# Kernel tuning notes

Hardware: AMD Instinct MI355X
Metric: run time of the kernel (lower is better)

## Reference

```python
import jax, jax.numpy as jnp
import numpy as np

L, B, D, H = 256, 128, 2048, 2048


def setup_inputs() -> dict:
    key = jax.random.key(0)
    k_x, k_ih, k_hh, k_b = jax.random.split(key, 4)
    scale_ih = 1.0 / np.sqrt(D)
    scale_hh = 1.0 / np.sqrt(H)
    return {
        "inputs": jax.random.normal(k_x, (L, B, D), dtype=jnp.float32),
        "W_ih": jax.random.normal(k_ih, (D, H), dtype=jnp.float32) * scale_ih,
        "W_hh": jax.random.normal(k_hh, (H, H), dtype=jnp.float32) * scale_hh,
        "b": jax.random.normal(k_b, (H,), dtype=jnp.float32) * scale_hh,
    }


def reference(inputs, W_ih, W_hh, b):
    """RNN.forward with a vanilla tanh cell, non-packed path, return_output=True.

    cell.forward(x, h) -> (h', h') with h' = tanh(x @ W_ih + h @ W_hh + b).
    default_state = zeros. Returns (stacked outputs [L,B,H], final state [B,H]).
    """
    # Hoist the input projection out of the scan (x @ W_ih is time-parallel).
    xp = jnp.einsum("lbd,dh->lbh", inputs, W_ih) + b  # [L, B, H]

    def step(h, x_t):
        h_new = jnp.tanh(x_t + h @ W_hh)  # [B, H]
        return h_new, h_new

    h0 = jnp.zeros((inputs.shape[1], W_hh.shape[0]), dtype=inputs.dtype)
    final_state, outputs = jax.lax.scan(step, h0, xp)
    return outputs, final_state
```

## Files before the change

kernel.cpp:

```cpp
#include <hip/hip_runtime.h>
#include <hip/hip_bf16.h>
#include <cmath>

#define LSEQ 256
#define BB   128
#define DD   2048
#define HH   2048
#define LB   (LSEQ * BB)
#define BH   (BB * HH)

typedef __attribute__((ext_vector_type(8))) short bf16x8;
typedef __attribute__((ext_vector_type(4))) float f32x4;

__device__ __forceinline__ void split2(float x, short& hi, short& lo) {
    unsigned u = __float_as_uint(x);
    hi = (short)(u >> 16);
    float r = x - __uint_as_float(u & 0xffff0000u);
    lo = (short)(__float_as_uint(r) >> 16);
}

__global__ __launch_bounds__(256) void xp_gemm(const float* __restrict__ A,
                                               const float* __restrict__ W,
                                               const float* __restrict__ bias,
                                               float* __restrict__ C) {
    __shared__ float As[128][33];
    __shared__ float Bs[128][33];

    const int tid  = threadIdx.x;
    const int lane = tid & 63;
    const int wave = tid >> 6;
    const int wm   = (wave >> 1) * 64;
    const int wn   = (wave & 1) * 64;
    const int l15  = lane & 15;
    const int lk   = (lane >> 4) * 8;

    const int row0 = blockIdx.x * 128;
    const int col0 = blockIdx.y * 128;

    f32x4 acc[4][4] = {};

    const int ar  = tid >> 3;
    const int ac4 = (tid & 7) * 4;
    const int bk  = tid >> 5;
    const int bc4 = (tid & 31) * 4;

    for (int k0 = 0; k0 < DD; k0 += 32) {
#pragma unroll
        for (int i = 0; i < 4; ++i) {
            const float4 v = *reinterpret_cast<const float4*>(
                &A[(size_t)(row0 + ar + 32 * i) * DD + k0 + ac4]);
            As[ar + 32 * i][ac4 + 0] = v.x;
            As[ar + 32 * i][ac4 + 1] = v.y;
            As[ar + 32 * i][ac4 + 2] = v.z;
            As[ar + 32 * i][ac4 + 3] = v.w;
        }
#pragma unroll
        for (int i = 0; i < 4; ++i) {
            const float4 v = *reinterpret_cast<const float4*>(
                &W[(size_t)(k0 + bk + 8 * i) * HH + col0 + bc4]);
            Bs[bc4 + 0][bk + 8 * i] = v.x;
            Bs[bc4 + 1][bk + 8 * i] = v.y;
            Bs[bc4 + 2][bk + 8 * i] = v.z;
            Bs[bc4 + 3][bk + 8 * i] = v.w;
        }
        __syncthreads();

        bf16x8 ah[4], al[4], bh[4], bl[4];
#pragma unroll
        for (int m = 0; m < 4; ++m) {
            const float* p = &As[wm + m * 16 + l15][lk];
#pragma unroll
            for (int j = 0; j < 8; ++j) {
                short h, l;
                split2(p[j], h, l);
                ah[m][j] = h; al[m][j] = l;
            }
        }
#pragma unroll
        for (int n = 0; n < 4; ++n) {
            const float* p = &Bs[wn + n * 16 + l15][lk];
#pragma unroll
            for (int j = 0; j < 8; ++j) {
                short h, l;
                split2(p[j], h, l);
                bh[n][j] = h; bl[n][j] = l;
            }
        }
#pragma unroll
        for (int m = 0; m < 4; ++m)
#pragma unroll
            for (int n = 0; n < 4; ++n) {
                acc[m][n] = __builtin_amdgcn_mfma_f32_16x16x32_bf16(ah[m], bh[n], acc[m][n], 0, 0, 0);
                acc[m][n] = __builtin_amdgcn_mfma_f32_16x16x32_bf16(ah[m], bl[n], acc[m][n], 0, 0, 0);
                acc[m][n] = __builtin_amdgcn_mfma_f32_16x16x32_bf16(al[m], bh[n], acc[m][n], 0, 0, 0);
            }
        __syncthreads();
    }

    const int r4 = (lane >> 4) * 4;
#pragma unroll
    for (int m = 0; m < 4; ++m)
#pragma unroll
        for (int n = 0; n < 4; ++n)
#pragma unroll
            for (int r = 0; r < 4; ++r) {
                const int row = row0 + wm + m * 16 + r4 + r;
                const int col = col0 + wn + n * 16 + l15;
                C[(size_t)row * HH + col] = acc[m][n][r] + bias[col];
            }
}

__global__ __launch_bounds__(256) void tanh0_kernel(float* __restrict__ out0) {
    const int i = blockIdx.x * 256 + threadIdx.x;
    float4* p = reinterpret_cast<float4*>(out0) + i;
    float4 v = *p;
    v.x = tanhf(v.x);
    v.y = tanhf(v.y);
    v.z = tanhf(v.z);
    v.w = tanhf(v.w);
    *p = v;
}

__global__ __launch_bounds__(256) void rnn_step(const float* __restrict__ hprev,
                                                const float* __restrict__ W,
                                                float* __restrict__ io) {
    __shared__ float As[4][32][33];
    __shared__ float Bs[4][32][33];
    __shared__ float red[4][32][33];

    const int tid  = threadIdx.x;
    const int lane = tid & 63;
    const int wave = tid >> 6;
    const int l15  = lane & 15;
    const int lk   = (lane >> 4) * 8;

    const int nc = blockIdx.x & 63;
    const int mr = blockIdx.x >> 6;
    const int m0 = mr * 32;
    const int n0 = nc * 32;

    const int r0 = lane >> 3;
    const int c4 = (lane & 7) * 4;

    f32x4 acc[2][2] = {};

    for (int kt = 0; kt < 16; ++kt) {
        const int k0 = wave * 512 + kt * 32;
#pragma unroll
        for (int i = 0; i < 4; ++i) {
            const float4 v = *reinterpret_cast<const float4*>(
                &hprev[(size_t)(m0 + r0 + 8 * i) * HH + k0 + c4]);
            As[wave][r0 + 8 * i][c4 + 0] = v.x;
            As[wave][r0 + 8 * i][c4 + 1] = v.y;
            As[wave][r0 + 8 * i][c4 + 2] = v.z;
            As[wave][r0 + 8 * i][c4 + 3] = v.w;
        }
#pragma unroll
        for (int i = 0; i < 4; ++i) {
            const float4 v = *reinterpret_cast<const float4*>(
                &W[(size_t)(k0 + r0 + 8 * i) * HH + n0 + c4]);
            Bs[wave][c4 + 0][r0 + 8 * i] = v.x;
            Bs[wave][c4 + 1][r0 + 8 * i] = v.y;
            Bs[wave][c4 + 2][r0 + 8 * i] = v.z;
            Bs[wave][c4 + 3][r0 + 8 * i] = v.w;
        }
        bf16x8 ah[2], al[2], bh[2], bl[2];
#pragma unroll
        for (int m = 0; m < 2; ++m) {
            const float* p = &As[wave][m * 16 + l15][lk];
#pragma unroll
            for (int j = 0; j < 8; ++j) {
                short h, l;
                split2(p[j], h, l);
                ah[m][j] = h; al[m][j] = l;
            }
        }
#pragma unroll
        for (int n = 0; n < 2; ++n) {
            const float* p = &Bs[wave][n * 16 + l15][lk];
#pragma unroll
            for (int j = 0; j < 8; ++j) {
                short h, l;
                split2(p[j], h, l);
                bh[n][j] = h; bl[n][j] = l;
            }
        }
#pragma unroll
        for (int m = 0; m < 2; ++m)
#pragma unroll
            for (int n = 0; n < 2; ++n) {
                acc[m][n] = __builtin_amdgcn_mfma_f32_16x16x32_bf16(ah[m], bh[n], acc[m][n], 0, 0, 0);
                acc[m][n] = __builtin_amdgcn_mfma_f32_16x16x32_bf16(ah[m], bl[n], acc[m][n], 0, 0, 0);
                acc[m][n] = __builtin_amdgcn_mfma_f32_16x16x32_bf16(al[m], bh[n], acc[m][n], 0, 0, 0);
            }
    }

    const int r4 = (lane >> 4) * 4;
#pragma unroll
    for (int m = 0; m < 2; ++m)
#pragma unroll
        for (int n = 0; n < 2; ++n)
#pragma unroll
            for (int r = 0; r < 4; ++r)
                red[wave][m * 16 + r4 + r][n * 16 + l15] = acc[m][n][r];
    __syncthreads();

    const int rr = tid >> 3;
    const int cc = (tid & 7) * 4;
    float* dst = &io[(size_t)(m0 + rr) * HH + n0 + cc];
    float4 xv = *reinterpret_cast<const float4*>(dst);
    float o0 = xv.x + red[0][rr][cc + 0] + red[1][rr][cc + 0] + red[2][rr][cc + 0] + red[3][rr][cc + 0];
    float o1 = xv.y + red[0][rr][cc + 1] + red[1][rr][cc + 1] + red[2][rr][cc + 1] + red[3][rr][cc + 1];
    float o2 = xv.z + red[0][rr][cc + 2] + red[1][rr][cc + 2] + red[2][rr][cc + 2] + red[3][rr][cc + 2];
    float o3 = xv.w + red[0][rr][cc + 3] + red[1][rr][cc + 3] + red[2][rr][cc + 3] + red[3][rr][cc + 3];
    float4 ov;
    ov.x = tanhf(o0);
    ov.y = tanhf(o1);
    ov.z = tanhf(o2);
    ov.w = tanhf(o3);
    *reinterpret_cast<float4*>(dst) = ov;
}

extern "C" void kernel_launch(void* const* d_in, const int* in_sizes, int n_in,
                              void* d_out, int out_size, void* d_ws, size_t ws_size,
                              hipStream_t stream) {
    (void)in_sizes; (void)n_in; (void)d_ws; (void)ws_size; (void)out_size;

    const float* X   = (const float*)d_in[0];
    const float* Wih = (const float*)d_in[1];
    const float* Whh = (const float*)d_in[2];
    const float* b   = (const float*)d_in[3];
    float* out = (float*)d_out;

    dim3 g1(LB / 128, HH / 128);
    xp_gemm<<<g1, 256, 0, stream>>>(X, Wih, b, out);

    tanh0_kernel<<<256, 256, 0, stream>>>(out);

    for (int t = 1; t < LSEQ; ++t) {
        rnn_step<<<256, 256, 0, stream>>>(out + (size_t)(t - 1) * BH, Whh,
                                          out + (size_t)t * BH);
    }

    hipMemcpyAsync(out + (size_t)LSEQ * BH, out + (size_t)(LSEQ - 1) * BH,
                   (size_t)BH * sizeof(float), hipMemcpyDeviceToDevice, stream);
}
```

Before: 5.111 ms.

## Pre-split weights into transposed bf16 hi/lo and carry split hidden state

Adds a pre-pass that transposes W_ih and W_hh and splits them into bf16 hi/lo halves in workspace, so the GEMMs load ready MFMA operands with global_load_lds instead of re-splitting fp32 every tile. The recurrent step now also writes the hi/lo split of the new hidden state into ping-pong buffers, so the next step reads bf16 operands directly. It also changes rnn_step tiling to 64x32 with 128 blocks, swizzles LDS for the input GEMM, and remaps the xp_gemm grid. The cost is two extra transpose kernels, extra global writes of the split state, and fewer blocks per step.

After: 6.997 ms. 36.9% more time.

```diff
diff --git a/kernel.cpp b/kernel.cpp
--- a/kernel.cpp
+++ b/kernel.cpp
@@ -6,10 +6,10 @@
 #define BB   128
 #define DD   2048
 #define HH   2048
-#define LB   (LSEQ * BB)
-#define BH   (BB * HH)
-
-typedef __attribute__((ext_vector_type(8))) short bf16x8;
+#define BH   (BB*HH)
+
+typedef __attribute__((ext_vector_type(8))) short short8;
+typedef __attribute__((ext_vector_type(4))) short short4v;
 typedef __attribute__((ext_vector_type(4))) float f32x4;
 
 __device__ __forceinline__ void split2(float x, short& hi, short& lo) {
@@ -19,72 +19,121 @@
     lo = (short)(__float_as_uint(r) >> 16);
 }
 
-__global__ __launch_bounds__(256) void xp_gemm(const float* __restrict__ A,
-                                               const float* __restrict__ W,
+__device__ __forceinline__ void g2l16(const void* g, void* l) {
+    __builtin_amdgcn_global_load_lds(
+        (const __attribute__((address_space(1))) unsigned int*)g,
+        (__attribute__((address_space(3))) unsigned int*)l, 16, 0, 0);
+}
+
+__global__ __launch_bounds__(256) void transpose_split(const float* __restrict__ W,
+                                                       short* __restrict__ outH,
+                                                       short* __restrict__ outL) {
+    __shared__ float S[64][65];
+    const int tid = threadIdx.x;
+    const int r0 = blockIdx.x * 64;
+    const int c0 = blockIdx.y * 64;
+    const int lr = tid >> 2;
+    const int lc = (tid & 3) * 16;
+#pragma unroll
+    for (int j = 0; j < 4; ++j) {
+        f32x4 v = *(const f32x4*)&W[(size_t)(r0 + lr) * DD + c0 + lc + 4*j];
+#pragma unroll
+        for (int q = 0; q < 4; ++q) S[lr][lc + 4*j + q] = v[q];
+    }
+    __syncthreads();
+    short8 h8[2], l8[2];
+#pragma unroll
+    for (int j = 0; j < 16; ++j) {
+        short h, l;
+        split2(S[lc + j][lr], h, l);
+        h8[j >> 3][j & 7] = h; l8[j >> 3][j & 7] = l;
+    }
+    const size_t o = (size_t)(c0 + lr) * DD + r0 + lc;
+    *(short8*)&outH[o]     = h8[0];
+    *(short8*)&outH[o + 8] = h8[1];
+    *(short8*)&outL[o]     = l8[0];
+    *(short8*)&outL[o + 8] = l8[1];
+}
+
+__global__ __launch_bounds__(256) void xp_gemm(const float* __restrict__ X,
+                                               const short* __restrict__ WTh,
+                                               const short* __restrict__ WTl,
                                                const float* __restrict__ bias,
                                                float* __restrict__ C) {
-    __shared__ float As[128][33];
-    __shared__ float Bs[128][33];
-
-    const int tid  = threadIdx.x;
-    const int lane = tid & 63;
-    const int wave = tid >> 6;
-    const int wm   = (wave >> 1) * 64;
-    const int wn   = (wave & 1) * 64;
-    const int l15  = lane & 15;
-    const int lk   = (lane >> 4) * 8;
-
-    const int row0 = blockIdx.x * 128;
-    const int col0 = blockIdx.y * 128;
+    __shared__ short Ah_s[128*32], Al_s[128*32];
+    __shared__ short Bh_s[128*32], Bl_s[128*32];
+
+    const int tid = threadIdx.x, lane = tid & 63, wave = tid >> 6;
+    const int l15 = lane & 15, lg = lane >> 4;
+
+    const int gid = blockIdx.x;
+    const int rt = ((gid >> 8) << 4) | (gid & 15);
+    const int ct = (gid >> 4) & 15;
+    const int row0 = rt * 128, col0 = ct * 128;
+
+    const int wm = (wave >> 1) * 64, wn = (wave & 1) * 64;
+
+    const int s_row = tid >> 1;
+    const float* gA = X + (size_t)(row0 + s_row) * DD + (tid & 1) * 16;
+    const int swzw = ((s_row >> 1) & 3) << 4;
+    char* pAh0 = (char*)Ah_s + s_row*64 + (((tid & 1)*32 +  0) ^ swzw);
+    char* pAh1 = (char*)Ah_s + s_row*64 + (((tid & 1)*32 + 16) ^ swzw);
+    char* pAl0 = (char*)Al_s + s_row*64 + (((tid & 1)*32 +  0) ^ swzw);
+    char* pAl1 = (char*)Al_s + s_row*64 + (((tid & 1)*32 + 16) ^ swzw);
+
+    const int brow = lane >> 2, bcol = (lane & 3) * 8;
+    const short* gBh = WTh + (size_t)(col0 + wave*32 + brow) * DD + bcol;
+    const short* gBl = WTl + (size_t)(col0 + wave*32 + brow) * DD + bcol;
+    short* lBh = &Bh_s[(wave*32)*32];
+    short* lBl = &Bl_s[(wave*32)*32];
+
+    int ra[4], rb[4];
+#pragma unroll
+    for (int m = 0; m < 4; ++m) {
+        const int rowm = wm + m*16 + l15;
+        ra[m] = rowm*64 + ((lg*16) ^ (((rowm >> 1) & 3) << 4));
+    }
+#pragma unroll
+    for (int n = 0; n < 4; ++n) {
+        const int rn = wn + n*16 + l15;
+        rb[n] = rn*64 + lg*16;
+    }
 
     f32x4 acc[4][4] = {};
 
-    const int ar  = tid >> 3;
-    const int ac4 = (tid & 7) * 4;
-    const int bk  = tid >> 5;
-    const int bc4 = (tid & 31) * 4;
-
     for (int k0 = 0; k0 < DD; k0 += 32) {
-#pragma unroll
-        for (int i = 0; i < 4; ++i) {
-            const float4 v = *reinterpret_cast<const float4*>(
-                &A[(size_t)(row0 + ar + 32 * i) * DD + k0 + ac4]);
-            As[ar + 32 * i][ac4 + 0] = v.x;
-            As[ar + 32 * i][ac4 + 1] = v.y;
-            As[ar + 32 * i][ac4 + 2] = v.z;
-            As[ar + 32 * i][ac4 + 3] = v.w;
-        }
-#pragma unroll
-        for (int i = 0; i < 4; ++i) {
-            const float4 v = *reinterpret_cast<const float4*>(
-                &W[(size_t)(k0 + bk + 8 * i) * HH + col0 + bc4]);
-            Bs[bc4 + 0][bk + 8 * i] = v.x;
-            Bs[bc4 + 1][bk + 8 * i] = v.y;
-            Bs[bc4 + 2][bk + 8 * i] = v.z;
-            Bs[bc4 + 3][bk + 8 * i] = v.w;
-        }
+        float xr[16];
+        *(f32x4*)&xr[0]  = *(const f32x4*)(gA + k0);
+        *(f32x4*)&xr[4]  = *(const f32x4*)(gA + k0 + 4);
+        *(f32x4*)&xr[8]  = *(const f32x4*)(gA + k0 + 8);
+        *(f32x4*)&xr[12] = *(const f32x4*)(gA + k0 + 12);
+
+        g2l16(gBh + k0,          lBh);
+        g2l16(gBh + k0 + 16*DD,  lBh + 16*32);
+        g2l16(gBl + k0,          lBl);
+        g2l16(gBl + k0 + 16*DD,  lBl + 16*32);
+
+        short8 vh0, vh1, vl0, vl1;
+#pragma unroll
+        for (int j = 0; j < 8; ++j) {
+            short h, l;
+            split2(xr[j], h, l);     vh0[j] = h; vl0[j] = l;
+            split2(xr[8+j], h, l);   vh1[j] = h; vl1[j] = l;
+        }
+        *(short8*)pAh0 = vh0; *(short8*)pAh1 = vh1;
+        *(short8*)pAl0 = vl0; *(short8*)pAl1 = vl1;
         __syncthreads();
 
-        bf16x8 ah[4], al[4], bh[4], bl[4];
+        short8 ah[4], al[4], bh[4], bl[4];
 #pragma unroll
         for (int m = 0; m < 4; ++m) {
-            const float* p = &As[wm + m * 16 + l15][lk];
-#pragma unroll
-            for (int j = 0; j < 8; ++j) {
-                short h, l;
-                split2(p[j], h, l);
-                ah[m][j] = h; al[m][j] = l;
-            }
+            ah[m] = *(const short8*)((const char*)Ah_s + ra[m]);
+            al[m] = *(const short8*)((const char*)Al_s + ra[m]);
         }
 #pragma unroll
         for (int n = 0; n < 4; ++n) {
-            const float* p = &Bs[wn + n * 16 + l15][lk];
-#pragma unroll
-            for (int j = 0; j < 8; ++j) {
-                short h, l;
-                split2(p[j], h, l);
-                bh[n][j] = h; bl[n][j] = l;
-            }
+            bh[n] = *(const short8*)((const char*)Bh_s + rb[n]);
+            bl[n] = *(const short8*)((const char*)Bl_s + rb[n]);
         }
 #pragma unroll
         for (int m = 0; m < 4; ++m)
@@ -97,134 +146,140 @@
         __syncthreads();
     }
 
-    const int r4 = (lane >> 4) * 4;
+    float bv[4];
+#pragma unroll
+    for (int n = 0; n < 4; ++n) bv[n] = bias[col0 + wn + n*16 + l15];
 #pragma unroll
     for (int m = 0; m < 4; ++m)
 #pragma unroll
         for (int n = 0; n < 4; ++n)
 #pragma unroll
-            for (int r = 0; r < 4; ++r) {
-                const int row = row0 + wm + m * 16 + r4 + r;
-                const int col = col0 + wn + n * 16 + l15;
-                C[(size_t)row * HH + col] = acc[m][n][r] + bias[col];
+            for (int i = 0; i < 4; ++i) {
+                const int row = row0 + wm + m*16 + lg*4 + i;
+                const int col = col0 + wn + n*16 + l15;
+                C[(size_t)row * HH + col] = acc[m][n][i] + bv[n];
             }
 }
 
-__global__ __launch_bounds__(256) void tanh0_kernel(float* __restrict__ out0) {
+__global__ __launch_bounds__(256) void tanh0_kernel(float* __restrict__ out0,
+                                                    short* __restrict__ oHi,
+                                                    short* __restrict__ oLo) {
     const int i = blockIdx.x * 256 + threadIdx.x;
-    float4* p = reinterpret_cast<float4*>(out0) + i;
-    float4 v = *p;
-    v.x = tanhf(v.x);
-    v.y = tanhf(v.y);
-    v.z = tanhf(v.z);
-    v.w = tanhf(v.w);
-    *p = v;
-}
-
-__global__ __launch_bounds__(256) void rnn_step(const float* __restrict__ hprev,
-                                                const float* __restrict__ W,
-                                                float* __restrict__ io) {
-    __shared__ float As[4][32][33];
-    __shared__ float Bs[4][32][33];
-    __shared__ float red[4][32][33];
-
-    const int tid  = threadIdx.x;
-    const int lane = tid & 63;
-    const int wave = tid >> 6;
-    const int l15  = lane & 15;
-    const int lk   = (lane >> 4) * 8;
-
-    const int nc = blockIdx.x & 63;
-    const int mr = blockIdx.x >> 6;
-    const int m0 = mr * 32;
-    const int n0 = nc * 32;
-
-    const int r0 = lane >> 3;
-    const int c4 = (lane & 7) * 4;
-
-    f32x4 acc[2][2] = {};
+    f32x4 v = ((const f32x4*)out0)[i];
+    short4v h4, l4;
+#pragma unroll
+    for (int q = 0; q < 4; ++q) {
+        const float t = tanhf(v[q]);
+        v[q] = t;
+        short h, l; split2(t, h, l);
+        h4[q] = h; l4[q] = l;
+    }
+    ((f32x4*)out0)[i]   = v;
+    ((short4v*)oHi)[i]  = h4;
+    ((short4v*)oLo)[i]  = l4;
+}
+
+__global__ __launch_bounds__(256) void rnn_step(const short* __restrict__ hHi,
+                                                const short* __restrict__ hLo,
+                                                const short* __restrict__ WTh,
+                                                const short* __restrict__ WTl,
+                                                float* __restrict__ io,
+                                                short* __restrict__ oHi,
+                                                short* __restrict__ oLo) {
+    __shared__ short Ah_s[4][64*32], Al_s[4][64*32];
+    __shared__ short Bh_s[4][32*32], Bl_s[4][32*32];
+    __shared__ float red[4][64*32];
+
+    const int tid = threadIdx.x, lane = tid & 63, wave = tid >> 6;
+    const int l15 = lane & 15, lg = lane >> 4;
+    const int mr = blockIdx.x & 1, nc = blockIdx.x >> 1;
+    const int m0 = mr * 64, n0 = nc * 32;
+
+    const int srow = lane >> 2, scol = (lane & 3) * 8;
+
+    const short* baseAh = hHi + (size_t)(m0 + srow) * HH + scol;
+    const short* baseAl = hLo + (size_t)(m0 + srow) * HH + scol;
+    const short* baseBh = WTh + (size_t)(n0 + srow) * HH + scol;
+    const short* baseBl = WTl + (size_t)(n0 + srow) * HH + scol;
+
+    f32x4 acc[4][2] = {};
 
     for (int kt = 0; kt < 16; ++kt) {
         const int k0 = wave * 512 + kt * 32;
 #pragma unroll
         for (int i = 0; i < 4; ++i) {
-            const float4 v = *reinterpret_cast<const float4*>(
-                &hprev[(size_t)(m0 + r0 + 8 * i) * HH + k0 + c4]);
-            As[wave][r0 + 8 * i][c4 + 0] = v.x;
-            As[wave][r0 + 8 * i][c4 + 1] = v.y;
-            As[wave][r0 + 8 * i][c4 + 2] = v.z;
-            As[wave][r0 + 8 * i][c4 + 3] = v.w;
-        }
-#pragma unroll
-        for (int i = 0; i < 4; ++i) {
-            const float4 v = *reinterpret_cast<const float4*>(
-                &W[(size_t)(k0 + r0 + 8 * i) * HH + n0 + c4]);
-            Bs[wave][c4 + 0][r0 + 8 * i] = v.x;
-            Bs[wave][c4 + 1][r0 + 8 * i] = v.y;
-            Bs[wave][c4 + 2][r0 + 8 * i] = v.z;
-            Bs[wave][c4 + 3][r0 + 8 * i] = v.w;
-        }
-        bf16x8 ah[2], al[2], bh[2], bl[2];
-#pragma unroll
-        for (int m = 0; m < 2; ++m) {
-            const float* p = &As[wave][m * 16 + l15][lk];
-#pragma unroll
-            for (int j = 0; j < 8; ++j) {
-                short h, l;
-                split2(p[j], h, l);
-                ah[m][j] = h; al[m][j] = l;
+            g2l16(baseAh + (size_t)i*16*HH + k0, &Ah_s[wave][i*16*32]);
+            g2l16(baseAl + (size_t)i*16*HH + k0, &Al_s[wave][i*16*32]);
+        }
+#pragma unroll
+        for (int i = 0; i < 2; ++i) {
+            g2l16(baseBh + (size_t)i*16*HH + k0, &Bh_s[wave][i*16*32]);
+            g2l16(baseBl + (size_t)i*16*HH + k0, &Bl_s[wave][i*16*32]);
+        }
+        __syncthreads();
+
+        short8 a_h[4], a_l[4], b_h[2], b_l[2];
+#pragma unroll
+        for (int m = 0; m < 4; ++m) {
+            a_h[m] = *(const short8*)&Ah_s[wave][(m*16 + l15)*32 + lg*8];
+            a_l[m] = *(const short8*)&Al_s[wave][(m*16 + l15)*32 + lg*8];
+        }
+#pragma unroll
+        for (int n = 0; n < 2; ++n) {
+            b_h[n] = *(const short8*)&Bh_s[wave][(n*16 + l15)*32 + lg*8];
+            b_l[n] = *(const short8*)&Bl_s[wave][(n*16 + l15)*32 + lg*8];
+        }
+#pragma unroll
+        for (int m = 0; m < 4; ++m)
+#pragma unroll
+            for (int n = 0; n < 2; ++n) {
+                acc[m][n] = __builtin_amdgcn_mfma_f32_16x16x32_bf16(a_h[m], b_h[n], acc[m][n], 0, 0, 0);
+                acc[m][n] = __builtin_amdgcn_mfma_f32_16x16x32_bf16(a_h[m], b_l[n], acc[m][n], 0, 0, 0);
+                acc[m][n] = __builtin_amdgcn_mfma_f32_16x16x32_bf16(a_l[m], b_h[n], acc[m][n], 0, 0, 0);
             }
-        }
-#pragma unroll
-        for (int n = 0; n < 2; ++n) {
-            const float* p = &Bs[wave][n * 16 + l15][lk];
-#pragma unroll
-            for (int j = 0; j < 8; ++j) {
-                short h, l;
-                split2(p[j], h, l);
-                bh[n][j] = h; bl[n][j] = l;
-            }
-        }
-#pragma unroll
-        for (int m = 0; m < 2; ++m)
-#pragma unroll
-            for (int n = 0; n < 2; ++n) {
-                acc[m][n] = __builtin_amdgcn_mfma_f32_16x16x32_bf16(ah[m], bh[n], acc[m][n], 0, 0, 0);
-                acc[m][n] = __builtin_amdgcn_mfma_f32_16x16x32_bf16(ah[m], bl[n], acc[m][n], 0, 0, 0);
-                acc[m][n] = __builtin_amdgcn_mfma_f32_16x16x32_bf16(al[m], bh[n], acc[m][n], 0, 0, 0);
-            }
-    }
-
-    const int r4 = (lane >> 4) * 4;
-#pragma unroll
-    for (int m = 0; m < 2; ++m)
+        __syncthreads();
+    }
+
+#pragma unroll
+    for (int m = 0; m < 4; ++m)
 #pragma unroll
         for (int n = 0; n < 2; ++n)
 #pragma unroll
-            for (int r = 0; r < 4; ++r)
-                red[wave][m * 16 + r4 + r][n * 16 + l15] = acc[m][n][r];
+            for (int i = 0; i < 4; ++i)
+                red[wave][(m*16 + lg*4 + i)*32 + n*16 + l15] = acc[m][n][i];
     __syncthreads();
 
-    const int rr = tid >> 3;
-    const int cc = (tid & 7) * 4;
-    float* dst = &io[(size_t)(m0 + rr) * HH + n0 + cc];
-    float4 xv = *reinterpret_cast<const float4*>(dst);
-    float o0 = xv.x + red[0][rr][cc + 0] + red[1][rr][cc + 0] + red[2][rr][cc + 0] + red[3][rr][cc + 0];
-    float o1 = xv.y + red[0][rr][cc + 1] + red[1][rr][cc + 1] + red[2][rr][cc + 1] + red[3][rr][cc + 1];
-    float o2 = xv.z + red[0][rr][cc + 2] + red[1][rr][cc + 2] + red[2][rr][cc + 2] + red[3][rr][cc + 2];
-    float o3 = xv.w + red[0][rr][cc + 3] + red[1][rr][cc + 3] + red[2][rr][cc + 3] + red[3][rr][cc + 3];
-    float4 ov;
-    ov.x = tanhf(o0);
-    ov.y = tanhf(o1);
-    ov.z = tanhf(o2);
-    ov.w = tanhf(o3);
-    *reinterpret_cast<float4*>(dst) = ov;
+    const int r = tid >> 2;
+    const int cb = (tid & 3) * 8;
+    float* dst = io + (size_t)(m0 + r) * HH + n0 + cb;
+    short4v h4[2], l4[2];
+#pragma unroll
+    for (int j = 0; j < 2; ++j) {
+        f32x4 xv = *(const f32x4*)(dst + j*4);
+        f32x4 ov;
+#pragma unroll
+        for (int q = 0; q < 4; ++q) {
+            const int c = cb + j*4 + q;
+            const float s = xv[q] + red[0][r*32 + c] + red[1][r*32 + c]
+                                  + red[2][r*32 + c] + red[3][r*32 + c];
+            const float t = tanhf(s);
+            ov[q] = t;
+            short h, l; split2(t, h, l);
+            h4[j][q] = h; l4[j][q] = l;
+        }
+        *(f32x4*)(dst + j*4) = ov;
+    }
+    const size_t po = (size_t)(m0 + r) * HH + n0 + cb;
+    *(short4v*)&oHi[po]     = h4[0];
+    *(short4v*)&oHi[po + 4] = h4[1];
+    *(short4v*)&oLo[po]     = l4[0];
+    *(short4v*)&oLo[po + 4] = l4[1];
 }
 
 extern "C" void kernel_launch(void* const* d_in, const int* in_sizes, int n_in,
                               void* d_out, int out_size, void* d_ws, size_t ws_size,
                               hipStream_t stream) {
-    (void)in_sizes; (void)n_in; (void)d_ws; (void)ws_size; (void)out_size;
+    (void)in_sizes; (void)n_in; (void)out_size; (void)ws_size;
 
     const float* X   = (const float*)d_in[0];
     const float* Wih = (const float*)d_in[1];
@@ -232,14 +287,28 @@
     const float* b   = (const float*)d_in[3];
     float* out = (float*)d_out;
 
-    dim3 g1(LB / 128, HH / 128);
-    xp_gemm<<<g1, 256, 0, stream>>>(X, Wih, b, out);
-
-    tanh0_kernel<<<256, 256, 0, stream>>>(out);
+    char* ws = (char*)d_ws;
+    short* WihTh = (short*)(ws);
+    short* WihTl = (short*)(ws + (size_t) 8*1024*1024);
+    short* WhhTh = (short*)(ws + (size_t)16*1024*1024);
+    short* WhhTl = (short*)(ws + (size_t)24*1024*1024);
+    short* hb[2][2];
+    hb[0][0] = (short*)(ws + (size_t)32*1024*1024);
+    hb[0][1] = (short*)(ws + (size_t)32*1024*1024 + 512*1024);
+    hb[1][0] = (short*)(ws + (size_t)33*1024*1024);
+    hb[1][1] = (short*)(ws + (size_t)33*1024*1024 + 512*1024);
+
+    dim3 tg(32, 32);
+    transpose_split<<<tg, 256, 0, stream>>>(Wih, WihTh, WihTl);
+    transpose_split<<<tg, 256, 0, stream>>>(Whh, WhhTh, WhhTl);
+
+    xp_gemm<<<4096, 256, 0, stream>>>(X, WihTh, WihTl, b, out);
+    tanh0_kernel<<<256, 256, 0, stream>>>(out, hb[0][0], hb[0][1]);
 
     for (int t = 1; t < LSEQ; ++t) {
-        rnn_step<<<256, 256, 0, stream>>>(out + (size_t)(t - 1) * BH, Whh,
-                                          out + (size_t)t * BH);
+        const int pi = (t - 1) & 1, po = t & 1;
+        rnn_step<<<128, 256, 0, stream>>>(hb[pi][0], hb[pi][1], WhhTh, WhhTl,
+                                          out + (size_t)t * BH, hb[po][0], hb[po][1]);
     }
 
     hipMemcpyAsync(out + (size_t)LSEQ * BH, out + (size_t)(LSEQ - 1) * BH,
```
